# Optimization experiments

Hardware: AMD Instinct MI355X
Metric: run time of the kernel (lower is better)

The kernel has to match this reference:

```python
import jax, jax.numpy as jnp
import numpy as np

N_NODES = 100000
N_EDGES = 1600000
IN_FEATS = 128
HIDDEN = 128
OUT_DIM = 128


def setup_inputs() -> dict:
    key = jax.random.key(0)
    ks = jax.random.split(key, 8)
    x = jax.random.normal(ks[0], (N_NODES, IN_FEATS), dtype=jnp.float32)
    W1 = jax.random.normal(ks[1], (IN_FEATS, HIDDEN), dtype=jnp.float32) * (1.0 / np.sqrt(IN_FEATS))
    b1 = jnp.zeros((HIDDEN,), dtype=jnp.float32)
    W2 = jax.random.normal(ks[2], (HIDDEN, HIDDEN), dtype=jnp.float32) * (1.0 / np.sqrt(HIDDEN))
    b2 = jnp.zeros((HIDDEN,), dtype=jnp.float32)
    W3 = jax.random.normal(ks[3], (HIDDEN, OUT_DIM), dtype=jnp.float32) * (1.0 / np.sqrt(HIDDEN))
    b3 = jnp.zeros((OUT_DIM,), dtype=jnp.float32)
    edge_src = jax.random.randint(ks[4], (N_EDGES,), 0, N_NODES, dtype=jnp.int32)
    edge_dst = jax.random.randint(ks[5], (N_EDGES,), 0, N_NODES, dtype=jnp.int32)
    return {"x": x, "W1": W1, "b1": b1, "W2": W2, "b2": b2, "W3": W3, "b3": b3,
            "edge_src": edge_src, "edge_dst": edge_dst}


def _mean_agg(h, edge_src, edge_dst, inv_deg):
    # gather src features, scatter-sum to dst, divide by in-degree (mean)
    summed = jax.ops.segment_sum(h[edge_src], edge_dst, num_segments=N_NODES)
    return summed * inv_deg[:, None]


def reference(x, W1, b1, W2, b2, W3, b3, edge_src, edge_dst):
    # in-degree (clamped to 1 to avoid div-by-zero, matching mean over empty = 0)
    deg = jax.ops.segment_sum(jnp.ones((N_EDGES,), dtype=jnp.float32), edge_dst,
                              num_segments=N_NODES)
    inv_deg = 1.0 / jnp.maximum(deg, 1.0)

    # DGL GINConv (eps=0, mean): h = Linear(h + mean_neighbors(h))
    h = x
    h = (h + _mean_agg(h, edge_src, edge_dst, inv_deg)) @ W1 + b1
    h = jax.nn.relu(h)  # dropout inactive in eval mode
    h = (h + _mean_agg(h, edge_src, edge_dst, inv_deg)) @ W2 + b2
    h = jax.nn.relu(h)
    h = (h + _mean_agg(h, edge_src, edge_dst, inv_deg)) @ W3 + b3
    return h
```

## Files before the change

### kernel.cpp

```cpp
#include <hip/hip_runtime.h>
#include <hip/hip_bf16.h>
#include <stdint.h>

#if __has_builtin(__builtin_amdgcn_cvt_pk_f32_fp8) && __has_builtin(__builtin_amdgcn_cvt_pk_fp8_f32)
#define FP8_HW 1
#else
#define FP8_HW 0
#include <hip/hip_fp8.h>
#endif

#define N_NODES 100000
#define N_EDGES 1600000
#define FEAT 128

#define BKT_SHIFT 8
#define BKT_SIZE  256
#define NB_BKT    391
#define BKT_CAP   5120
#define NB_SC     800
#define EPB_SC    2000

typedef uint16_t u16;
typedef uint32_t u32;
typedef __attribute__((ext_vector_type(8))) short bf16x8;
typedef __attribute__((ext_vector_type(4))) float f32x4;
typedef __attribute__((ext_vector_type(2))) float f32x2;

__device__ __forceinline__ u16 bf16_rn(float f){
  u32 u = __float_as_uint(f);
  u += 0x7FFFu + ((u >> 16) & 1u);
  return (u16)(u >> 16);
}
__device__ __forceinline__ float bf16_lo(u32 p){ return __uint_as_float(p << 16); }
__device__ __forceinline__ float bf16_hi(u32 p){ return __uint_as_float(p & 0xFFFF0000u); }

__device__ __forceinline__ void fp8x4_to_f32(u32 w, float* o){
#if FP8_HW
  f32x2 a = __builtin_amdgcn_cvt_pk_f32_fp8(w, false);
  f32x2 b = __builtin_amdgcn_cvt_pk_f32_fp8(w, true);
  o[0] = a.x; o[1] = a.y; o[2] = b.x; o[3] = b.y;
#else
  #pragma unroll
  for (int i = 0; i < 4; ++i){
    __hip_fp8_e4m3 t; t.__x = (uint8_t)((w >> (8 * i)) & 0xFF);
    o[i] = (float)t;
  }
#endif
}
__device__ __forceinline__ u32 f32x4_to_fp8(float a, float b, float c, float d){
#if FP8_HW
  u32 r = __builtin_amdgcn_cvt_pk_fp8_f32(a, b, 0, false);
  r = __builtin_amdgcn_cvt_pk_fp8_f32(c, d, r, true);
  return r;
#else
  __hip_fp8_e4m3 qa(a), qb(b), qc(c), qd(d);
  return (u32)qa.__x | ((u32)qb.__x << 8) | ((u32)qc.__x << 16) | ((u32)qd.__x << 24);
#endif
}


__global__ __launch_bounds__(512) void hist_kernel(const int* __restrict__ dst,
                                                   int* __restrict__ hcnt){
  __shared__ int h[NB_BKT];
  for (int i = threadIdx.x; i < NB_BKT; i += 512) h[i] = 0;
  __syncthreads();
  int base = blockIdx.x * EPB_SC;
  for (int e = base + threadIdx.x; e < base + EPB_SC; e += 512)
    atomicAdd(&h[dst[e] >> BKT_SHIFT], 1);
  __syncthreads();
  for (int i = threadIdx.x; i < NB_BKT; i += 512)
    hcnt[blockIdx.x * NB_BKT + i] = h[i];
}

__global__ void hscan_kernel(int* __restrict__ hcnt, int* __restrict__ cursor){
  __shared__ int s[256];
  int b = blockIdx.x, t = threadIdx.x;
  int v[4]; int sum = 0;
  #pragma unroll
  for (int j = 0; j < 4; ++j){
    int blk = 4 * t + j;
    v[j] = (blk < NB_SC) ? hcnt[blk * NB_BKT + b] : 0;
    sum += v[j];
  }
  s[t] = sum;
  __syncthreads();
  for (int d = 1; d < 256; d <<= 1){
    int add = (t >= d) ? s[t - d] : 0;
    __syncthreads();
    s[t] += add;
    __syncthreads();
  }
  int excl = s[t] - sum;
  #pragma unroll
  for (int j = 0; j < 4; ++j){
    int blk = 4 * t + j;
    if (blk < NB_SC){ hcnt[blk * NB_BKT + b] = excl; excl += v[j]; }
  }
  if (t == 255) cursor[b] = s[255];
}

__global__ __launch_bounds__(512) void scatter_kernel(const int* __restrict__ src,
                                                      const int* __restrict__ dst,
                                                      const int* __restrict__ hcnt,
                                                      uint2* __restrict__ bbuf){
  __shared__ int cur[NB_BKT];
  for (int i = threadIdx.x; i < NB_BKT; i += 512)
    cur[i] = hcnt[blockIdx.x * NB_BKT + i];
  __syncthreads();
  int base = blockIdx.x * EPB_SC;
  for (int e = base + threadIdx.x; e < base + EPB_SC; e += 512){
    int d = dst[e];
    int b = d >> BKT_SHIFT;
    int p = atomicAdd(&cur[b], 1);
    bbuf[(size_t)b * BKT_CAP + p] = make_uint2((u32)src[e], (u32)(d & (BKT_SIZE - 1)));
  }
}

__global__ __launch_bounds__(1024) void csr_build_kernel(const uint2* __restrict__ bbuf,
                                 const int* __restrict__ cursor,
                                 int* __restrict__ offs, int* __restrict__ deg,
                                 float* __restrict__ inv_deg, int* __restrict__ eidx){
  __shared__ int hist[BKT_SIZE];
  __shared__ int s[BKT_SIZE];
  __shared__ int cu[BKT_SIZE];
  int b = blockIdx.x;
  int t = threadIdx.x;
  int lo = b * BKT_CAP;
  int hi = lo + cursor[b];
  if (t < BKT_SIZE) hist[t] = 0;
  __syncthreads();
  for (int e = lo + t; e < hi; e += 1024)
    atomicAdd(&hist[bbuf[e].y], 1);
  __syncthreads();
  int v = 0, pv = 0;
  if (t < BKT_SIZE){
    v  = hist[t];
    pv = (v + 3) & ~3;
    s[t] = pv;
  }
  __syncthreads();
  for (int d = 1; d < BKT_SIZE; d <<= 1){
    int add = (t < BKT_SIZE && t >= d) ? s[t - d] : 0;
    __syncthreads();
    if (t < BKT_SIZE && t >= d) s[t] += add;
    __syncthreads();
  }
  if (t < BKT_SIZE){
    int excl = s[t] - pv;
    int node = b * BKT_SIZE + t;
    if (node < N_NODES){
      offs[node]    = lo + excl;
      deg[node]     = v;
      inv_deg[node] = 1.0f / fmaxf((float)v, 1.0f);
    }
    s[t]  = excl;
    cu[t] = 0;
  }
  __syncthreads();
  for (int e = lo + t; e < hi; e += 1024){
    uint2 q = bbuf[e];
    int p = atomicAdd(&cu[q.y], 1);
    eidx[lo + s[q.y] + p] = (int)q.x;
  }
}


__global__ void cvt_x8_kernel(const float* __restrict__ x, uint2* __restrict__ X8){
  int i = blockIdx.x * 256 + threadIdx.x;
  const float4* p = (const float4*)x + (size_t)i * 2;
  float4 a = p[0], b = p[1];
  uint2 o;
  o.x = f32x4_to_fp8(a.x, a.y, a.z, a.w);
  o.y = f32x4_to_fp8(b.x, b.y, b.z, b.w);
  X8[i] = o;
}

__global__ void cvt_h8_kernel(const u16* __restrict__ H, uint2* __restrict__ H8){
  int i = blockIdx.x * 256 + threadIdx.x;
  uint4 hq = ((const uint4*)H)[i];
  uint2 o;
  o.x = f32x4_to_fp8(bf16_lo(hq.x), bf16_hi(hq.x), bf16_lo(hq.y), bf16_hi(hq.y));
  o.y = f32x4_to_fp8(bf16_lo(hq.z), bf16_hi(hq.z), bf16_lo(hq.w), bf16_hi(hq.w));
  H8[i] = o;
}

__global__ void wprep3_kernel(const float* __restrict__ W1, const float* __restrict__ W2,
                              const float* __restrict__ W3, u16* __restrict__ Wp1,
                              u16* __restrict__ Wp2, u16* __restrict__ Wp3){
  int which = blockIdx.x >> 6;
  int b     = blockIdx.x & 63;
  const float* W = (which == 0) ? W1 : (which == 1) ? W2 : W3;
  u16*        Wp = (which == 0) ? Wp1 : (which == 1) ? Wp2 : Wp3;
  int idx = b * 256 + threadIdx.x;
  int j    = idx & 7;
  int lane = (idx >> 3) & 63;
  int t    = idx >> 9;
  int k0 = t & 3, n0 = t >> 2;
  int k = k0 * 32 + (lane >> 4) * 8 + j;
  int n = n0 * 16 + (lane & 15);
  Wp[idx] = bf16_rn(W[k * FEAT + n]);
}

template<int SM>
__global__ void agg16_kernel(const u32* __restrict__ n8,
                             const u16* __restrict__ hb,
                             const float* __restrict__ xf,
                             const int* __restrict__ offs,
                             const int* __restrict__ deg,
                             const float* __restrict__ inv_deg,
                             const int* __restrict__ eidx,
                             u16* __restrict__ T){
  int wid   = (int)((blockIdx.x * 256u + threadIdx.x) >> 6);
  int lane  = threadIdx.x & 63;
  int nsub  = lane >> 4;
  int slice = lane & 15;
  int node  = wid * 4 + nsub;
  bool vn   = node < N_NODES;
  int nc    = vn ? node : 0;
  int start = offs[nc];
  int cnt   = vn ? deg[nc] : 0;
  const int* ep = eidx + start;

  float acc[8];
  #pragma unroll
  for (int j = 0; j < 8; ++j) acc[j] = 0.f;

  uint4 q = (cnt > 0) ? *(const uint4*)ep : make_uint4(0, 0, 0, 0);

  for (int e = 0; e < cnt; e += 4){
    uint4 qn = *(const uint4*)(ep + e + 4);
    int i0 = (int)q.x, i1 = (int)q.y, i2 = (int)q.z, i3 = (int)q.w;
    float f0 = 1.f;
    float f1 = (e + 1 < cnt) ? 1.f : 0.f; if (e + 1 >= cnt) i1 = 0;
    float f2 = (e + 2 < cnt) ? 1.f : 0.f; if (e + 2 >= cnt) i2 = 0;
    float f3 = (e + 3 < cnt) ? 1.f : 0.f; if (e + 3 >= cnt) i3 = 0;
    uint2 r0 = *(const uint2*)(n8 + (size_t)i0 * 32 + slice * 2);
    uint2 r1 = *(const uint2*)(n8 + (size_t)i1 * 32 + slice * 2);
    uint2 r2 = *(const uint2*)(n8 + (size_t)i2 * 32 + slice * 2);
    uint2 r3 = *(const uint2*)(n8 + (size_t)i3 * 32 + slice * 2);
    float t0[4], t1[4];
    fp8x4_to_f32(r0.x, t0); fp8x4_to_f32(r0.y, t1);
    acc[0]+=f0*t0[0]; acc[1]+=f0*t0[1]; acc[2]+=f0*t0[2]; acc[3]+=f0*t0[3];
    acc[4]+=f0*t1[0]; acc[5]+=f0*t1[1]; acc[6]+=f0*t1[2]; acc[7]+=f0*t1[3];
    fp8x4_to_f32(r1.x, t0); fp8x4_to_f32(r1.y, t1);
    acc[0]+=f1*t0[0]; acc[1]+=f1*t0[1]; acc[2]+=f1*t0[2]; acc[3]+=f1*t0[3];
    acc[4]+=f1*t1[0]; acc[5]+=f1*t1[1]; acc[6]+=f1*t1[2]; acc[7]+=f1*t1[3];
    fp8x4_to_f32(r2.x, t0); fp8x4_to_f32(r2.y, t1);
    acc[0]+=f2*t0[0]; acc[1]+=f2*t0[1]; acc[2]+=f2*t0[2]; acc[3]+=f2*t0[3];
    acc[4]+=f2*t1[0]; acc[5]+=f2*t1[1]; acc[6]+=f2*t1[2]; acc[7]+=f2*t1[3];
    fp8x4_to_f32(r3.x, t0); fp8x4_to_f32(r3.y, t1);
    acc[0]+=f3*t0[0]; acc[1]+=f3*t0[1]; acc[2]+=f3*t0[2]; acc[3]+=f3*t0[3];
    acc[4]+=f3*t1[0]; acc[5]+=f3*t1[1]; acc[6]+=f3*t1[2]; acc[7]+=f3*t1[3];
    q = qn;
  }

  if (!vn) return;
  float w = inv_deg[node];
  float self[8];
  if (SM == 1){
    const float* sp = xf + (size_t)node * FEAT + slice * 8;
    float4 a = *(const float4*)sp;
    float4 b = *(const float4*)(sp + 4);
    self[0]=a.x; self[1]=a.y; self[2]=a.z; self[3]=a.w;
    self[4]=b.x; self[5]=b.y; self[6]=b.z; self[7]=b.w;
  } else {
    const u16* sp = hb + (size_t)node * FEAT + slice * 8;
    uint4 s0 = *(const uint4*)sp;
    self[0]=bf16_lo(s0.x); self[1]=bf16_hi(s0.x); self[2]=bf16_lo(s0.y); self[3]=bf16_hi(s0.y);
    self[4]=bf16_lo(s0.z); self[5]=bf16_hi(s0.z); self[6]=bf16_lo(s0.w); self[7]=bf16_hi(s0.w);
  }
  uint4 o;
  o.x = (u32)bf16_rn(self[0] + w*acc[0]) | ((u32)bf16_rn(self[1] + w*acc[1]) << 16);
  o.y = (u32)bf16_rn(self[2] + w*acc[2]) | ((u32)bf16_rn(self[3] + w*acc[3]) << 16);
  o.z = (u32)bf16_rn(self[4] + w*acc[4]) | ((u32)bf16_rn(self[5] + w*acc[5]) << 16);
  o.w = (u32)bf16_rn(self[6] + w*acc[6]) | ((u32)bf16_rn(self[7] + w*acc[7]) << 16);
  *(uint4*)(T + (size_t)node * FEAT + slice * 8) = o;
}

template<int MODE>
__global__ __launch_bounds__(256) void gemm2_kernel(const u16* __restrict__ T,
                                                    const u16* __restrict__ Wp,
                                                    const float* __restrict__ bias,
                                                    void* __restrict__ out){
  int wave = threadIdx.x >> 6;
  int lane = threadIdx.x & 63;
  int row0 = blockIdx.x * 128 + wave * 32;
  if (row0 >= N_NODES) return;
  int quad = lane >> 4;
  int c    = lane & 15;

  f32x4 acc[2][8];
  #pragma unroll
  for (int t = 0; t < 2; ++t)
    #pragma unroll
    for (int i = 0; i < 8; ++i) acc[t][i] = (f32x4){0.f, 0.f, 0.f, 0.f};

  bf16x8 A[2][4];
  const u16* ar0 = T + (size_t)(row0 + c) * FEAT + quad * 8;
  const u16* ar1 = ar0 + 16 * FEAT;
  #pragma unroll
  for (int k0 = 0; k0 < 4; ++k0){
    A[0][k0] = *(const bf16x8*)(ar0 + k0 * 32);
    A[1][k0] = *(const bf16x8*)(ar1 + k0 * 32);
  }

  #pragma unroll
  for (int n0 = 0; n0 < 8; ++n0){
    #pragma unroll
    for (int k0 = 0; k0 < 4; ++k0){
      bf16x8 b = *(const bf16x8*)(Wp + (((n0 << 2) | k0) * 64 + lane) * 8);
      acc[0][n0] = __builtin_amdgcn_mfma_f32_16x16x32_bf16(A[0][k0], b, acc[0][n0], 0, 0, 0);
      acc[1][n0] = __builtin_amdgcn_mfma_f32_16x16x32_bf16(A[1][k0], b, acc[1][n0], 0, 0, 0);
    }
  }

  #pragma unroll
  for (int t = 0; t < 2; ++t){
    #pragma unroll
    for (int n0 = 0; n0 < 8; ++n0){
      float bv = bias[n0 * 16 + c];
      #pragma unroll
      for (int r = 0; r < 4; ++r){
        int row = row0 + t * 16 + quad * 4 + r;
        int col = n0 * 16 + c;
        float v = acc[t][n0][r] + bv;
        if (MODE == 0){
          v = fmaxf(v, 0.f);
          ((u16*)out)[(size_t)row * FEAT + col] = bf16_rn(v);
        } else {
          ((float*)out)[(size_t)row * FEAT + col] = v;
        }
      }
    }
  }
}


static inline size_t align_up(size_t x){ return (x + 255) & ~(size_t)255; }

extern "C" void kernel_launch(void* const* d_in, const int* in_sizes, int n_in,
                              void* d_out, int out_size, void* d_ws, size_t ws_size,
                              hipStream_t stream){
  const float* x  = (const float*)d_in[0];
  const float* W1 = (const float*)d_in[1];
  const float* b1 = (const float*)d_in[2];
  const float* W2 = (const float*)d_in[3];
  const float* b2 = (const float*)d_in[4];
  const float* W3 = (const float*)d_in[5];
  const float* b3 = (const float*)d_in[6];
  const int* esrc = (const int*)d_in[7];
  const int* edst = (const int*)d_in[8];

  char* w = (char*)d_ws;
  int*   cursor  = (int*)w;    w += align_up((size_t)NB_BKT * 4);
  int*   hcnt    = (int*)w;    w += align_up((size_t)NB_SC * NB_BKT * 4);
  int*   deg     = (int*)w;    w += align_up((size_t)N_NODES * 4);
  int*   offs    = (int*)w;    w += align_up((size_t)N_NODES * 4);
  float* inv_deg = (float*)w;  w += align_up((size_t)N_NODES * 4);
  int*   eidx    = (int*)w;    w += align_up((size_t)NB_BKT * BKT_CAP * 4);
  u16*   Wp1     = (u16*)w;    w += align_up((size_t)16384 * 2);
  u16*   Wp2     = (u16*)w;    w += align_up((size_t)16384 * 2);
  u16*   Wp3     = (u16*)w;    w += align_up((size_t)16384 * 2);
  u16*   T       = (u16*)w;    w += align_up((size_t)N_NODES * FEAT * 2);

  uint2* bbuf = (uint2*)T;

  u16* H  = (u16*)d_out;
  u32* H8 = (u32*)((char*)d_out + (size_t)N_NODES * FEAT * 2);
  u32* X8 = (u32*)((char*)d_out + (size_t)N_NODES * FEAT * 3);

  hist_kernel<<<NB_SC, 512, 0, stream>>>(edst, hcnt);
  hscan_kernel<<<NB_BKT, 256, 0, stream>>>(hcnt, cursor);
  scatter_kernel<<<NB_SC, 512, 0, stream>>>(esrc, edst, hcnt, bbuf);
  csr_build_kernel<<<NB_BKT, 1024, 0, stream>>>(bbuf, cursor, offs, deg, inv_deg, eidx);

  wprep3_kernel<<<192, 256, 0, stream>>>(W1, W2, W3, Wp1, Wp2, Wp3);
  cvt_x8_kernel<<<N_EDGES / 256, 256, 0, stream>>>(x, (uint2*)X8);

  const int AGG_BLOCKS  = (N_NODES + 15) / 16;
  const int GEMM_BLOCKS = (N_NODES + 127) / 128;
  const int CVT_BLOCKS  = N_EDGES / 256;

  agg16_kernel<1><<<AGG_BLOCKS, 256, 0, stream>>>(X8, (const u16*)nullptr, x,
                                                  offs, deg, inv_deg, eidx, T);
  gemm2_kernel<0><<<GEMM_BLOCKS, 256, 0, stream>>>(T, Wp1, b1, H);

  cvt_h8_kernel<<<CVT_BLOCKS, 256, 0, stream>>>(H, (uint2*)H8);
  agg16_kernel<0><<<AGG_BLOCKS, 256, 0, stream>>>(H8, H, (const float*)nullptr,
                                                  offs, deg, inv_deg, eidx, T);
  gemm2_kernel<0><<<GEMM_BLOCKS, 256, 0, stream>>>(T, Wp2, b2, H);

  cvt_h8_kernel<<<CVT_BLOCKS, 256, 0, stream>>>(H, (uint2*)H8);
  agg16_kernel<0><<<AGG_BLOCKS, 256, 0, stream>>>(H8, H, (const float*)nullptr,
                                                  offs, deg, inv_deg, eidx, T);
  gemm2_kernel<1><<<GEMM_BLOCKS, 256, 0, stream>>>(T, Wp3, b3, d_out);

  (void)in_sizes; (void)n_in; (void)out_size; (void)ws_size; (void)w;
}
```

Baseline: 334.1 us.

## Fuse aggregation, GEMM, and FP8 conversion into one per-layer kernel

Each GIN layer now runs as a single kernel. A 512-thread block aggregates 128 nodes into a swizzled shared-memory tile, runs the MFMA GEMM from that tile, and writes both the bf16 activations and their FP8 copy for the next layer. This removes the global round trip of the intermediate T buffer and the separate cvt_h8 passes, leaving three launches where there were nine. The cost is a 32KB shared tile and 512-thread blocks, which lowers occupancy for the latency-bound gather phase, and ping-pong buffers in the workspace.

Measured after the change: 339.9 us. No clear change (+1.7%).

```diff
diff --git a/kernel.cpp b/kernel.cpp
--- a/kernel.cpp
+++ b/kernel.cpp
@@ -173,15 +173,6 @@
   o.x = f32x4_to_fp8(a.x, a.y, a.z, a.w);
   o.y = f32x4_to_fp8(b.x, b.y, b.z, b.w);
   X8[i] = o;
-}
-
-__global__ void cvt_h8_kernel(const u16* __restrict__ H, uint2* __restrict__ H8){
-  int i = blockIdx.x * 256 + threadIdx.x;
-  uint4 hq = ((const uint4*)H)[i];
-  uint2 o;
-  o.x = f32x4_to_fp8(bf16_lo(hq.x), bf16_hi(hq.x), bf16_lo(hq.y), bf16_hi(hq.y));
-  o.y = f32x4_to_fp8(bf16_lo(hq.z), bf16_hi(hq.z), bf16_lo(hq.w), bf16_hi(hq.w));
-  H8[i] = o;
 }
 
 __global__ void wprep3_kernel(const float* __restrict__ W1, const float* __restrict__ W2,
@@ -201,135 +192,157 @@
   Wp[idx] = bf16_rn(W[k * FEAT + n]);
 }
 
-template<int SM>
-__global__ void agg16_kernel(const u32* __restrict__ n8,
-                             const u16* __restrict__ hb,
-                             const float* __restrict__ xf,
-                             const int* __restrict__ offs,
-                             const int* __restrict__ deg,
-                             const float* __restrict__ inv_deg,
-                             const int* __restrict__ eidx,
-                             u16* __restrict__ T){
-  int wid   = (int)((blockIdx.x * 256u + threadIdx.x) >> 6);
-  int lane  = threadIdx.x & 63;
-  int nsub  = lane >> 4;
-  int slice = lane & 15;
-  int node  = wid * 4 + nsub;
-  bool vn   = node < N_NODES;
-  int nc    = vn ? node : 0;
-  int start = offs[nc];
-  int cnt   = vn ? deg[nc] : 0;
-  const int* ep = eidx + start;
-
-  float acc[8];
-  #pragma unroll
-  for (int j = 0; j < 8; ++j) acc[j] = 0.f;
-
-  uint4 q = (cnt > 0) ? *(const uint4*)ep : make_uint4(0, 0, 0, 0);
-
-  for (int e = 0; e < cnt; e += 4){
-    uint4 qn = *(const uint4*)(ep + e + 4);
-    int i0 = (int)q.x, i1 = (int)q.y, i2 = (int)q.z, i3 = (int)q.w;
-    float f0 = 1.f;
-    float f1 = (e + 1 < cnt) ? 1.f : 0.f; if (e + 1 >= cnt) i1 = 0;
-    float f2 = (e + 2 < cnt) ? 1.f : 0.f; if (e + 2 >= cnt) i2 = 0;
-    float f3 = (e + 3 < cnt) ? 1.f : 0.f; if (e + 3 >= cnt) i3 = 0;
-    uint2 r0 = *(const uint2*)(n8 + (size_t)i0 * 32 + slice * 2);
-    uint2 r1 = *(const uint2*)(n8 + (size_t)i1 * 32 + slice * 2);
-    uint2 r2 = *(const uint2*)(n8 + (size_t)i2 * 32 + slice * 2);
-    uint2 r3 = *(const uint2*)(n8 + (size_t)i3 * 32 + slice * 2);
-    float t0[4], t1[4];
-    fp8x4_to_f32(r0.x, t0); fp8x4_to_f32(r0.y, t1);
-    acc[0]+=f0*t0[0]; acc[1]+=f0*t0[1]; acc[2]+=f0*t0[2]; acc[3]+=f0*t0[3];
-    acc[4]+=f0*t1[0]; acc[5]+=f0*t1[1]; acc[6]+=f0*t1[2]; acc[7]+=f0*t1[3];
-    fp8x4_to_f32(r1.x, t0); fp8x4_to_f32(r1.y, t1);
-    acc[0]+=f1*t0[0]; acc[1]+=f1*t0[1]; acc[2]+=f1*t0[2]; acc[3]+=f1*t0[3];
-    acc[4]+=f1*t1[0]; acc[5]+=f1*t1[1]; acc[6]+=f1*t1[2]; acc[7]+=f1*t1[3];
-    fp8x4_to_f32(r2.x, t0); fp8x4_to_f32(r2.y, t1);
-    acc[0]+=f2*t0[0]; acc[1]+=f2*t0[1]; acc[2]+=f2*t0[2]; acc[3]+=f2*t0[3];
-    acc[4]+=f2*t1[0]; acc[5]+=f2*t1[1]; acc[6]+=f2*t1[2]; acc[7]+=f2*t1[3];
-    fp8x4_to_f32(r3.x, t0); fp8x4_to_f32(r3.y, t1);
-    acc[0]+=f3*t0[0]; acc[1]+=f3*t0[1]; acc[2]+=f3*t0[2]; acc[3]+=f3*t0[3];
-    acc[4]+=f3*t1[0]; acc[5]+=f3*t1[1]; acc[6]+=f3*t1[2]; acc[7]+=f3*t1[3];
-    q = qn;
-  }
-
-  if (!vn) return;
-  float w = inv_deg[node];
-  float self[8];
-  if (SM == 1){
-    const float* sp = xf + (size_t)node * FEAT + slice * 8;
-    float4 a = *(const float4*)sp;
-    float4 b = *(const float4*)(sp + 4);
-    self[0]=a.x; self[1]=a.y; self[2]=a.z; self[3]=a.w;
-    self[4]=b.x; self[5]=b.y; self[6]=b.z; self[7]=b.w;
-  } else {
-    const u16* sp = hb + (size_t)node * FEAT + slice * 8;
-    uint4 s0 = *(const uint4*)sp;
-    self[0]=bf16_lo(s0.x); self[1]=bf16_hi(s0.x); self[2]=bf16_lo(s0.y); self[3]=bf16_hi(s0.y);
-    self[4]=bf16_lo(s0.z); self[5]=bf16_hi(s0.z); self[6]=bf16_lo(s0.w); self[7]=bf16_hi(s0.w);
-  }
-  uint4 o;
-  o.x = (u32)bf16_rn(self[0] + w*acc[0]) | ((u32)bf16_rn(self[1] + w*acc[1]) << 16);
-  o.y = (u32)bf16_rn(self[2] + w*acc[2]) | ((u32)bf16_rn(self[3] + w*acc[3]) << 16);
-  o.z = (u32)bf16_rn(self[4] + w*acc[4]) | ((u32)bf16_rn(self[5] + w*acc[5]) << 16);
-  o.w = (u32)bf16_rn(self[6] + w*acc[6]) | ((u32)bf16_rn(self[7] + w*acc[7]) << 16);
-  *(uint4*)(T + (size_t)node * FEAT + slice * 8) = o;
-}
-
-template<int MODE>
-__global__ __launch_bounds__(256) void gemm2_kernel(const u16* __restrict__ T,
-                                                    const u16* __restrict__ Wp,
-                                                    const float* __restrict__ bias,
-                                                    void* __restrict__ out){
-  int wave = threadIdx.x >> 6;
-  int lane = threadIdx.x & 63;
-  int row0 = blockIdx.x * 128 + wave * 32;
-  if (row0 >= N_NODES) return;
-  int quad = lane >> 4;
-  int c    = lane & 15;
-
-  f32x4 acc[2][8];
-  #pragma unroll
-  for (int t = 0; t < 2; ++t)
+
+template<int SM, int OUT>
+__global__ __launch_bounds__(512, 4) void layer_kernel(
+    const u32* __restrict__ n8,
+    const u16* __restrict__ hb,
+    const float* __restrict__ xf,
+    const int* __restrict__ offs,
+    const int* __restrict__ deg,
+    const float* __restrict__ inv_deg,
+    const int* __restrict__ eidx,
+    const u16* __restrict__ Wp,
+    const float* __restrict__ bias,
+    u16* __restrict__ Hout,
+    u32* __restrict__ H8out,
+    float* __restrict__ Fout){
+  __shared__ u16 Tt[128 * FEAT];
+  const int tid   = threadIdx.x;
+  const int wid   = tid >> 6;
+  const int lane  = tid & 63;
+  const int nsub  = lane >> 4;
+  const int slice = lane & 15;
+  const int base  = blockIdx.x * 128;
+
+  for (int g = 0; g < 4; ++g){
+    int rrow  = wid * 16 + g * 4 + nsub;
+    int node  = base + rrow;
+    bool vn   = node < N_NODES;
+    int nc    = vn ? node : 0;
+    int start = offs[nc];
+    int cnt   = vn ? deg[nc] : 0;
+    const int* ep = eidx + start;
+
+    float acc[8];
     #pragma unroll
-    for (int i = 0; i < 8; ++i) acc[t][i] = (f32x4){0.f, 0.f, 0.f, 0.f};
-
-  bf16x8 A[2][4];
-  const u16* ar0 = T + (size_t)(row0 + c) * FEAT + quad * 8;
-  const u16* ar1 = ar0 + 16 * FEAT;
+    for (int j = 0; j < 8; ++j) acc[j] = 0.f;
+
+    uint4 q = (cnt > 0) ? *(const uint4*)ep : make_uint4(0, 0, 0, 0);
+
+    for (int e = 0; e < cnt; e += 4){
+      uint4 qn = *(const uint4*)(ep + e + 4);
+      int i0 = (int)q.x, i1 = (int)q.y, i2 = (int)q.z, i3 = (int)q.w;
+      float f0 = 1.f;
+      float f1 = (e + 1 < cnt) ? 1.f : 0.f; if (e + 1 >= cnt) i1 = 0;
+      float f2 = (e + 2 < cnt) ? 1.f : 0.f; if (e + 2 >= cnt) i2 = 0;
+      float f3 = (e + 3 < cnt) ? 1.f : 0.f; if (e + 3 >= cnt) i3 = 0;
+      uint2 r0 = *(const uint2*)(n8 + (size_t)i0 * 32 + slice * 2);
+      uint2 r1 = *(const uint2*)(n8 + (size_t)i1 * 32 + slice * 2);
+      uint2 r2 = *(const uint2*)(n8 + (size_t)i2 * 32 + slice * 2);
+      uint2 r3 = *(const uint2*)(n8 + (size_t)i3 * 32 + slice * 2);
+      float t0[4], t1[4];
+      fp8x4_to_f32(r0.x, t0); fp8x4_to_f32(r0.y, t1);
+      acc[0]+=f0*t0[0]; acc[1]+=f0*t0[1]; acc[2]+=f0*t0[2]; acc[3]+=f0*t0[3];
+      acc[4]+=f0*t1[0]; acc[5]+=f0*t1[1]; acc[6]+=f0*t1[2]; acc[7]+=f0*t1[3];
+      fp8x4_to_f32(r1.x, t0); fp8x4_to_f32(r1.y, t1);
+      acc[0]+=f1*t0[0]; acc[1]+=f1*t0[1]; acc[2]+=f1*t0[2]; acc[3]+=f1*t0[3];
+      acc[4]+=f1*t1[0]; acc[5]+=f1*t1[1]; acc[6]+=f1*t1[2]; acc[7]+=f1*t1[3];
+      fp8x4_to_f32(r2.x, t0); fp8x4_to_f32(r2.y, t1);
+      acc[0]+=f2*t0[0]; acc[1]+=f2*t0[1]; acc[2]+=f2*t0[2]; acc[3]+=f2*t0[3];
+      acc[4]+=f2*t1[0]; acc[5]+=f2*t1[1]; acc[6]+=f2*t1[2]; acc[7]+=f2*t1[3];
+      fp8x4_to_f32(r3.x, t0); fp8x4_to_f32(r3.y, t1);
+      acc[0]+=f3*t0[0]; acc[1]+=f3*t0[1]; acc[2]+=f3*t0[2]; acc[3]+=f3*t0[3];
+      acc[4]+=f3*t1[0]; acc[5]+=f3*t1[1]; acc[6]+=f3*t1[2]; acc[7]+=f3*t1[3];
+      q = qn;
+    }
+
+    uint4 o = make_uint4(0, 0, 0, 0);
+    if (vn){
+      float w = inv_deg[node];
+      float self[8];
+      if (SM == 1){
+        const float* sp = xf + (size_t)node * FEAT + slice * 8;
+        float4 a = *(const float4*)sp;
+        float4 b = *(const float4*)(sp + 4);
+        self[0]=a.x; self[1]=a.y; self[2]=a.z; self[3]=a.w;
+        self[4]=b.x; self[5]=b.y; self[6]=b.z; self[7]=b.w;
+      } else {
+        const u16* sp = hb + (size_t)node * FEAT + slice * 8;
+        uint4 s0 = *(const uint4*)sp;
+        self[0]=bf16_lo(s0.x); self[1]=bf16_hi(s0.x); self[2]=bf16_lo(s0.y); self[3]=bf16_hi(s0.y);
+        self[4]=bf16_lo(s0.z); self[5]=bf16_hi(s0.z); self[6]=bf16_lo(s0.w); self[7]=bf16_hi(s0.w);
+      }
+      o.x = (u32)bf16_rn(self[0] + w*acc[0]) | ((u32)bf16_rn(self[1] + w*acc[1]) << 16);
+      o.y = (u32)bf16_rn(self[2] + w*acc[2]) | ((u32)bf16_rn(self[3] + w*acc[3]) << 16);
+      o.z = (u32)bf16_rn(self[4] + w*acc[4]) | ((u32)bf16_rn(self[5] + w*acc[5]) << 16);
+      o.w = (u32)bf16_rn(self[6] + w*acc[6]) | ((u32)bf16_rn(self[7] + w*acc[7]) << 16);
+    }
+    ((uint4*)Tt)[rrow * 16 + (slice ^ (rrow & 7))] = o;
+  }
+  __syncthreads();
+
+  const int quad = lane >> 4;
+  const int c    = lane & 15;
+  const int r0   = wid * 16;
+
+  bf16x8 A[4];
   #pragma unroll
   for (int k0 = 0; k0 < 4; ++k0){
-    A[0][k0] = *(const bf16x8*)(ar0 + k0 * 32);
-    A[1][k0] = *(const bf16x8*)(ar1 + k0 * 32);
-  }
+    uint4 t = ((const uint4*)Tt)[(r0 + c) * 16 + ((quad + k0 * 4) ^ ((r0 + c) & 7))];
+    A[k0] = *(const bf16x8*)&t;
+  }
+
+  f32x4 acc2[8];
+  #pragma unroll
+  for (int i = 0; i < 8; ++i) acc2[i] = (f32x4){0.f, 0.f, 0.f, 0.f};
 
   #pragma unroll
   for (int n0 = 0; n0 < 8; ++n0){
     #pragma unroll
     for (int k0 = 0; k0 < 4; ++k0){
-      bf16x8 b = *(const bf16x8*)(Wp + (((n0 << 2) | k0) * 64 + lane) * 8);
-      acc[0][n0] = __builtin_amdgcn_mfma_f32_16x16x32_bf16(A[0][k0], b, acc[0][n0], 0, 0, 0);
-      acc[1][n0] = __builtin_amdgcn_mfma_f32_16x16x32_bf16(A[1][k0], b, acc[1][n0], 0, 0, 0);
-    }
-  }
-
-  #pragma unroll
-  for (int t = 0; t < 2; ++t){
+      bf16x8 b = *(const bf16x8*)(Wp + (size_t)(((n0 << 2) | k0) * 64 + lane) * 8);
+      acc2[n0] = __builtin_amdgcn_mfma_f32_16x16x32_bf16(A[k0], b, acc2[n0], 0, 0, 0);
+    }
+  }
+
+  if (OUT == 1){
     #pragma unroll
     for (int n0 = 0; n0 < 8; ++n0){
       float bv = bias[n0 * 16 + c];
       #pragma unroll
       for (int r = 0; r < 4; ++r){
-        int row = row0 + t * 16 + quad * 4 + r;
+        int row = base + r0 + quad * 4 + r;
+        if (row < N_NODES)
+          Fout[(size_t)row * FEAT + n0 * 16 + c] = acc2[n0][r] + bv;
+      }
+    }
+  } else {
+    __syncthreads();
+    #pragma unroll
+    for (int n0 = 0; n0 < 8; ++n0){
+      float bv = bias[n0 * 16 + c];
+      #pragma unroll
+      for (int r = 0; r < 4; ++r){
+        int rr  = r0 + quad * 4 + r;
         int col = n0 * 16 + c;
-        float v = acc[t][n0][r] + bv;
-        if (MODE == 0){
-          v = fmaxf(v, 0.f);
-          ((u16*)out)[(size_t)row * FEAT + col] = bf16_rn(v);
-        } else {
-          ((float*)out)[(size_t)row * FEAT + col] = v;
-        }
+        float v = fmaxf(acc2[n0][r] + bv, 0.f);
+        Tt[rr * FEAT + (col ^ ((rr & 7) << 3))] = bf16_rn(v);
+      }
+    }
+    __syncthreads();
+    #pragma unroll
+    for (int it = 0; it < 4; ++it){
+      int p  = it * 512 + tid;
+      int rr = p >> 4, qq = p & 15;
+      int node = base + rr;
+      if (node < N_NODES){
+        uint4 d = ((const uint4*)Tt)[rr * 16 + (qq ^ (rr & 7))];
+        *(uint4*)(Hout + (size_t)node * FEAT + qq * 8) = d;
+        uint2 o8;
+        o8.x = f32x4_to_fp8(bf16_lo(d.x), bf16_hi(d.x), bf16_lo(d.y), bf16_hi(d.y));
+        o8.y = f32x4_to_fp8(bf16_lo(d.z), bf16_hi(d.z), bf16_lo(d.w), bf16_hi(d.w));
+        *(uint2*)(H8out + (size_t)node * 32 + qq * 2) = o8;
       }
     }
   }
@@ -361,13 +374,14 @@
   u16*   Wp1     = (u16*)w;    w += align_up((size_t)16384 * 2);
   u16*   Wp2     = (u16*)w;    w += align_up((size_t)16384 * 2);
   u16*   Wp3     = (u16*)w;    w += align_up((size_t)16384 * 2);
-  u16*   T       = (u16*)w;    w += align_up((size_t)N_NODES * FEAT * 2);
-
-  uint2* bbuf = (uint2*)T;
-
-  u16* H  = (u16*)d_out;
-  u32* H8 = (u32*)((char*)d_out + (size_t)N_NODES * FEAT * 2);
-  u32* X8 = (u32*)((char*)d_out + (size_t)N_NODES * FEAT * 3);
+  u16*   Hb      = (u16*)w;    w += align_up((size_t)N_NODES * FEAT * 2);
+  u32*   H8b     = (u32*)w;    w += align_up((size_t)N_NODES * 32 * 4);
+
+  uint2* bbuf = (uint2*)Hb;
+
+  u16* Ha  = (u16*)d_out;
+  u32* H8a = (u32*)((char*)d_out + (size_t)N_NODES * FEAT * 2);
+  u32* X8  = (u32*)((char*)d_out + (size_t)N_NODES * FEAT * 3);
 
   hist_kernel<<<NB_SC, 512, 0, stream>>>(edst, hcnt);
   hscan_kernel<<<NB_BKT, 256, 0, stream>>>(hcnt, cursor);
@@ -377,23 +391,19 @@
   wprep3_kernel<<<192, 256, 0, stream>>>(W1, W2, W3, Wp1, Wp2, Wp3);
   cvt_x8_kernel<<<N_EDGES / 256, 256, 0, stream>>>(x, (uint2*)X8);
 
-  const int AGG_BLOCKS  = (N_NODES + 15) / 16;
-  const int GEMM_BLOCKS = (N_NODES + 127) / 128;
-  const int CVT_BLOCKS  = N_EDGES / 256;
-
-  agg16_kernel<1><<<AGG_BLOCKS, 256, 0, stream>>>(X8, (const u16*)nullptr, x,
-                                                  offs, deg, inv_deg, eidx, T);
-  gemm2_kernel<0><<<GEMM_BLOCKS, 256, 0, stream>>>(T, Wp1, b1, H);
-
-  cvt_h8_kernel<<<CVT_BLOCKS, 256, 0, stream>>>(H, (uint2*)H8);
-  agg16_kernel<0><<<AGG_BLOCKS, 256, 0, stream>>>(H8, H, (const float*)nullptr,
-                                                  offs, deg, inv_deg, eidx, T);
-  gemm2_kernel<0><<<GEMM_BLOCKS, 256, 0, stream>>>(T, Wp2, b2, H);
-
-  cvt_h8_kernel<<<CVT_BLOCKS, 256, 0, stream>>>(H, (uint2*)H8);
-  agg16_kernel<0><<<AGG_BLOCKS, 256, 0, stream>>>(H8, H, (const float*)nullptr,
-                                                  offs, deg, inv_deg, eidx, T);
-  gemm2_kernel<1><<<GEMM_BLOCKS, 256, 0, stream>>>(T, Wp3, b3, d_out);
+  const int LAYER_BLOCKS = (N_NODES + 127) / 128;
+
+  layer_kernel<1, 0><<<LAYER_BLOCKS, 512, 0, stream>>>(
+      X8, (const u16*)nullptr, x, offs, deg, inv_deg, eidx, Wp1, b1,
+      Ha, H8a, (float*)nullptr);
+
+  layer_kernel<0, 0><<<LAYER_BLOCKS, 512, 0, stream>>>(
+      H8a, Ha, (const float*)nullptr, offs, deg, inv_deg, eidx, Wp2, b2,
+      Hb, H8b, (float*)nullptr);
+
+  layer_kernel<0, 1><<<LAYER_BLOCKS, 512, 0, stream>>>(
+      H8b, Hb, (const float*)nullptr, offs, deg, inv_deg, eidx, Wp3, b3,
+      (u16*)nullptr, (u32*)nullptr, (float*)d_out);
 
   (void)in_sizes; (void)n_in; (void)out_size; (void)ws_size; (void)w;
 }
```
